# Performance work log

Measured on AMD Instinct MI355X. Metric: run time of the kernel, lower is better.

The kernel has to match this reference:

```python
import jax, jax.numpy as jnp
import numpy as np

N_NODES = 100000
N_EDGES = 500000
NUM_REL = 1000  # static stand-in for rel.max()+1 (all relation ids appear w.h.p.)
E_HID, T_HID, R_HID = 256, 128, 128
NEG_SLOPE = 0.01  # F.leaky_relu default


def setup_inputs() -> dict:
    key = jax.random.key(0)
    ks = jax.random.split(key, 8)
    x_e = jax.random.normal(ks[0], (N_NODES, E_HID), dtype=jnp.float32)
    edge_index = jax.random.randint(ks[1], (2, N_EDGES), 0, N_NODES, dtype=jnp.int32)
    rel = jax.random.randint(ks[2], (N_EDGES,), 0, NUM_REL, dtype=jnp.int32)
    x_res1 = jax.random.normal(ks[3], (N_EDGES, R_HID), dtype=jnp.float32)
    rel_size = jnp.arange(N_EDGES, dtype=jnp.int32)  # column indices of the spmm
    s = 0.02
    W_tc1 = jax.random.normal(ks[4], (E_HID, T_HID), dtype=jnp.float32) * s
    b_tc1 = jnp.zeros((T_HID,), dtype=jnp.float32)
    W_sr1 = jax.random.normal(ks[5], (2 * T_HID, R_HID), dtype=jnp.float32) * s
    b_sr1 = jnp.zeros((R_HID,), dtype=jnp.float32)
    a1 = jax.random.normal(ks[6], (R_HID,), dtype=jnp.float32) * s
    a5 = jax.random.normal(ks[7], (R_HID,), dtype=jnp.float32) * s
    return {"x_e": x_e, "x_res1": x_res1, "W_tc1": W_tc1, "b_tc1": b_tc1,
            "W_sr1": W_sr1, "b_sr1": b_sr1, "a1": a1, "a5": a5,
            "edge_index": edge_index, "rel": rel, "rel_size": rel_size}


def reference(x_e, x_res1, W_tc1, b_tc1, W_sr1, b_sr1, a1, a5, edge_index, rel, rel_size):
    # t_c1: project node features to t_hidden
    s_t = x_e @ W_tc1 + b_tc1                      # [N, t]
    h = s_t[edge_index[0]]                          # [E, t] head features
    t = s_t[edge_index[1]]                          # [E, t] tail features

    # Per-relation mean of head/tail features (in torch this overwrites r_in_t,
    # which aliases r_in_t1, so downstream uses the means).
    counts = jax.ops.segment_sum(jnp.ones_like(rel, dtype=jnp.float32), rel,
                                 num_segments=NUM_REL)
    denom = jnp.maximum(counts, 1.0)[:, None]       # [R, 1]
    mean_h = jax.ops.segment_sum(h, rel, num_segments=NUM_REL) / denom  # [R, t]
    mean_t = jax.ops.segment_sum(t, rel, num_segments=NUM_REL) / denom  # [R, t]
    r_in_t1 = jnp.concatenate([mean_h[rel], mean_t[rel]], axis=1)       # [E, 2t]

    # s_r1 projection and attention logits
    x_res2 = r_in_t1 @ W_sr1 + b_sr1                # [E, r]
    e1 = x_res2 @ a1 + x_res1 @ a5                  # [E]
    e1 = jnp.where(e1 >= 0, e1, NEG_SLOPE * e1)     # leaky_relu

    # scatter-softmax grouped by rel
    seg_max = jax.ops.segment_max(e1, rel, num_segments=NUM_REL)
    ex = jnp.exp(e1 - seg_max[rel])
    seg_sum = jax.ops.segment_sum(ex, rel, num_segments=NUM_REL)
    alpha = ex / seg_sum[rel]                       # [E]

    # spmm: sparse [R, E] with (row=rel, col=rel_size, val=alpha) times x_res2
    x_type = jax.ops.segment_sum(alpha[:, None] * x_res2[rel_size], rel,
                                 num_segments=NUM_REL)  # [R, r]

    out_res = x_res1 + x_type[rel]                  # [E, r]
    return jnp.concatenate([out_res, r_in_t1], axis=1)  # [E, r + 2t]
```

## Files before the change

kernel.cpp:

```cpp
#include <hip/hip_runtime.h>

#define N_NODES_C 100000
#define N_EDGES_C 500000
#define NUM_REL_C 1000
#define E_HID_C   256
#define RPAD      1024

#define NB_SORT   125
#define CHUNK_E   (N_EDGES_C / NB_SORT)


__global__ __launch_bounds__(1024)
void k_zero(int* __restrict__ cnt) {
    cnt[threadIdx.x] = 0;
}

__global__ __launch_bounds__(1024)
void k_hist(const int* __restrict__ rel, int* __restrict__ part,
            int* __restrict__ cnt) {
    __shared__ int h[RPAD];
    const int b = blockIdx.x, tid = threadIdx.x;
    h[tid] = 0;
    __syncthreads();
    const int base = b * CHUNK_E;
    for (int e = base + tid; e < base + CHUNK_E; e += 1024)
        atomicAdd(&h[rel[e]], 1);
    __syncthreads();
    const int v = h[tid];
    part[b * RPAD + tid] = v;
    if (v) atomicAdd(&cnt[tid], v);
}

__global__ __launch_bounds__(1024)
void k_scan(const int* __restrict__ cnt, int* __restrict__ startc) {
    __shared__ int s[2][RPAD];
    const int t = threadIdx.x;
    const int v = cnt[t];
    s[0][t] = v;
    __syncthreads();
    int cur = 0;
    for (int off = 1; off < RPAD; off <<= 1) {
        const int add = (t >= off) ? s[cur][t - off] : 0;
        s[cur ^ 1][t] = s[cur][t] + add;
        cur ^= 1;
        __syncthreads();
    }
    startc[t] = s[cur][t] - v;
}

__global__ __launch_bounds__(64)
void k_pbase(const int* __restrict__ part, const int* __restrict__ startc,
             int* __restrict__ pbase) {
    const int r = blockIdx.x * 64 + threadIdx.x;
    int run = startc[r];
#pragma unroll 5
    for (int b = 0; b < NB_SORT; ++b) {
        pbase[b * RPAD + r] = run;
        run += part[b * RPAD + r];
    }
}

__global__ __launch_bounds__(1024)
void k_scatter(const int* __restrict__ edge_index, const int* __restrict__ rel,
               const int* __restrict__ pbase,
               int* __restrict__ bsrc, int* __restrict__ bdst) {
    __shared__ int cur[RPAD];
    const int b = blockIdx.x, tid = threadIdx.x;
    cur[tid] = pbase[b * RPAD + tid];
    __syncthreads();
    const int base = b * CHUNK_E;
    for (int e = base + tid; e < base + CHUNK_E; e += 1024) {
        const int r = rel[e];
        const int pos = atomicAdd(&cur[r], 1);
        bsrc[pos] = edge_index[e];
        bdst[pos] = edge_index[N_EDGES_C + e];
    }
}

__global__ __launch_bounds__(512)
void k_accum(const float* __restrict__ x_e,
             const int* __restrict__ bsrc, const int* __restrict__ bdst,
             const int* __restrict__ startc, const int* __restrict__ cnt,
             const float* __restrict__ W_tc1, const float* __restrict__ b_tc1,
             const float* __restrict__ W_sr1, const float* __restrict__ b_sr1,
             float* __restrict__ rin_t,
             float* __restrict__ xt_t)
{
    __shared__ float red[8][E_HID_C];
    __shared__ float mh[E_HID_C], mt[E_HID_C], rin[E_HID_C];
    const int r    = blockIdx.x;
    const int tid  = threadIdx.x;
    const int w    = tid >> 6;
    const int lane = tid & 63;
    const int which = w >> 2;
    const int q     = w & 3;
    const int base = startc[r];
    const int c    = cnt[r];
    const int qlen = (c + 3) >> 2;
    const int lo = base + q * qlen;
    const int hi = min(base + c, lo + qlen);
    const int* __restrict__ bn = which ? bdst : bsrc;

    float4 a = make_float4(0.f, 0.f, 0.f, 0.f);
    for (int g = lo; g < hi; g += 64) {
        const int m = min(64, hi - g);
        const int myidx = (g + lane < hi) ? bn[g + lane] : 0;
        int k = 0;
        for (; k + 8 <= m; k += 8) {
            float4 v[8];
#pragma unroll
            for (int u = 0; u < 8; ++u) {
                const int n = __shfl(myidx, k + u);
                v[u] = ((const float4*)(x_e + (size_t)n * E_HID_C))[lane];
            }
#pragma unroll
            for (int u = 0; u < 8; ++u) {
                a.x += v[u].x; a.y += v[u].y; a.z += v[u].z; a.w += v[u].w;
            }
        }
        for (; k < m; ++k) {
            const int n = __shfl(myidx, k);
            const float4 v = ((const float4*)(x_e + (size_t)n * E_HID_C))[lane];
            a.x += v.x; a.y += v.y; a.z += v.z; a.w += v.w;
        }
    }

    ((float4*)&red[w][0])[lane] = a;
    __syncthreads();

    {
        const float inv = 1.0f / (float)(c > 0 ? c : 1);
        const int wh = tid >> 8;
        const int d  = tid & 255;
        const float s = red[wh * 4 + 0][d] + red[wh * 4 + 1][d] +
                        red[wh * 4 + 2][d] + red[wh * 4 + 3][d];
        (wh ? mt : mh)[d] = s * inv;
    }
    __syncthreads();

    if (tid < 256) {
        const int j = tid & 127;
        const float* __restrict__ src = (tid < 128) ? mh : mt;
        float acc = b_tc1[j];
        for (int k = 0; k < E_HID_C; ++k)
            acc += src[k] * W_tc1[k * 128 + j];
        rin[(tid < 128 ? 0 : 128) + j] = acc;
    }
    __syncthreads();

    if (tid < 256) {
        rin_t[(size_t)r * E_HID_C + tid] = rin[tid];
    } else if (tid < 384) {
        const int d = tid - 256;
        float acc = b_sr1[d];
        for (int k = 0; k < E_HID_C; ++k)
            acc += rin[k] * W_sr1[k * 128 + d];
        xt_t[(size_t)r * 128 + d] = acc;
    }
}

__global__ __launch_bounds__(256)
void k_out(const float* __restrict__ x_res1,
           const int* __restrict__ rel,
           const float* __restrict__ rin_t,
           const float* __restrict__ xt_t,
           float4* __restrict__ out)
{
    const float4* __restrict__ xr4  = (const float4*)x_res1;
    const float4* __restrict__ rin4 = (const float4*)rin_t;
    const float4* __restrict__ xt4  = (const float4*)xt_t;
    const int tid = threadIdx.x;
    const unsigned jj = tid & 31;
    const unsigned e  = blockIdx.x * 8u + (tid >> 5);
    const int r = rel[e];
    const float4 a = xr4[(size_t)e * 32 + jj];
    const float4 t = xt4[(size_t)r * 32 + jj];
    float4 o;
    o.x = a.x + t.x; o.y = a.y + t.y; o.z = a.z + t.z; o.w = a.w + t.w;
    float4* __restrict__ dst = out + (size_t)e * 96;
    dst[jj]      = o;
    dst[32 + jj] = rin4[(size_t)r * 64 + jj];
    dst[64 + jj] = rin4[(size_t)r * 64 + 32 + jj];
}

extern "C" void kernel_launch(void* const* d_in, const int* in_sizes, int n_in,
                              void* d_out, int out_size, void* d_ws, size_t ws_size,
                              hipStream_t stream)
{
    const float* x_e    = (const float*)d_in[0];
    const float* x_res1 = (const float*)d_in[1];
    const float* W_tc1  = (const float*)d_in[2];
    const float* b_tc1  = (const float*)d_in[3];
    const float* W_sr1  = (const float*)d_in[4];
    const float* b_sr1  = (const float*)d_in[5];
    const int* edge_index = (const int*)d_in[8];
    const int* rel        = (const int*)d_in[9];

    char* ws = (char*)d_ws;
    int*   part   = (int*)  (ws);
    int*   pbase  = (int*)  (ws + 512000);
    int*   cnt    = (int*)  (ws + 1024000);
    int*   startc = (int*)  (ws + 1028096);
    int*   bsrc   = (int*)  (ws + 1032192);
    int*   bdst   = (int*)  (ws + 3032192);
    float* rin_t  = (float*)(ws + 5032192);
    float* xt_t   = (float*)(ws + 6056192);

    k_zero   <<<1, RPAD, 0, stream>>>(cnt);
    k_hist   <<<NB_SORT, 1024, 0, stream>>>(rel, part, cnt);
    k_scan   <<<1, RPAD, 0, stream>>>(cnt, startc);
    k_pbase  <<<RPAD / 64, 64, 0, stream>>>(part, startc, pbase);
    k_scatter<<<NB_SORT, 1024, 0, stream>>>(edge_index, rel, pbase, bsrc, bdst);
    k_accum  <<<NUM_REL_C, 512, 0, stream>>>(x_e, bsrc, bdst, startc, cnt,
                                             W_tc1, b_tc1, W_sr1, b_sr1,
                                             rin_t, xt_t);
    k_out    <<<N_EDGES_C / 8, 256, 0, stream>>>(x_res1, rel, rin_t, xt_t,
                                                 (float4*)d_out);
}
```

Measured before the change: 381.8 us.

## Gather bf16 copy of node features, pack edge pairs, nontemporal output

Converts x_e to bf16 inside the histogram kernel when workspace allows, so the per-relation gather reads half the bytes per row; the gather unroll also grows from 8 to 16. Source and destination indices are packed into one int2 array, and the output kernel uses nontemporal loads and stores. The conversion is an extra full streaming pass over x_e (about 102 MB read, 51 MB written) that must be paid back by the cheaper random gathers. Summing bf16-rounded inputs also loses precision in the means.

```diff
diff --git a/kernel.cpp b/kernel.cpp
--- a/kernel.cpp
+++ b/kernel.cpp
@@ -8,7 +8,18 @@
 
 #define NB_SORT   125
 #define CHUNK_E   (N_EDGES_C / NB_SORT)
-
+#define NB_HIST   250
+#define XE_F4     (N_NODES_C * E_HID_C / 4)
+#define CONV_PER_BLK (XE_F4 / NB_HIST)
+
+
+typedef float f4 __attribute__((ext_vector_type(4)));
+
+__device__ __forceinline__ unsigned short bf16rne(float f) {
+    unsigned u = __float_as_uint(f);
+    u += 0x7FFFu + ((u >> 16) & 1u);
+    return (unsigned short)(u >> 16);
+}
 
 __global__ __launch_bounds__(1024)
 void k_zero(int* __restrict__ cnt) {
@@ -16,19 +27,35 @@
 }
 
 __global__ __launch_bounds__(1024)
-void k_hist(const int* __restrict__ rel, int* __restrict__ part,
-            int* __restrict__ cnt) {
+void k_hist(const int* __restrict__ rel, const float4* __restrict__ xe4,
+            int* __restrict__ part, int* __restrict__ cnt,
+            ushort4* __restrict__ xb4, const int do_conv) {
     __shared__ int h[RPAD];
     const int b = blockIdx.x, tid = threadIdx.x;
-    h[tid] = 0;
-    __syncthreads();
-    const int base = b * CHUNK_E;
-    for (int e = base + tid; e < base + CHUNK_E; e += 1024)
-        atomicAdd(&h[rel[e]], 1);
-    __syncthreads();
-    const int v = h[tid];
-    part[b * RPAD + tid] = v;
-    if (v) atomicAdd(&cnt[tid], v);
+    const bool hist = (b < NB_SORT);
+    if (hist) {
+        h[tid] = 0;
+        __syncthreads();
+        const int base = b * CHUNK_E;
+        for (int e = base + tid; e < base + CHUNK_E; e += 1024)
+            atomicAdd(&h[rel[e]], 1);
+    }
+    if (do_conv) {
+        const int cb = b * CONV_PER_BLK;
+        for (int i = cb + tid; i < cb + CONV_PER_BLK; i += 1024) {
+            const float4 v = xe4[i];
+            ushort4 o;
+            o.x = bf16rne(v.x); o.y = bf16rne(v.y);
+            o.z = bf16rne(v.z); o.w = bf16rne(v.w);
+            xb4[i] = o;
+        }
+    }
+    if (hist) {
+        __syncthreads();
+        const int c = h[tid];
+        part[b * RPAD + tid] = c;
+        if (c) atomicAdd(&cnt[tid], c);
+    }
 }
 
 __global__ __launch_bounds__(1024)
@@ -62,8 +89,7 @@
 
 __global__ __launch_bounds__(1024)
 void k_scatter(const int* __restrict__ edge_index, const int* __restrict__ rel,
-               const int* __restrict__ pbase,
-               int* __restrict__ bsrc, int* __restrict__ bdst) {
+               const int* __restrict__ pbase, int2* __restrict__ bpair) {
     __shared__ int cur[RPAD];
     const int b = blockIdx.x, tid = threadIdx.x;
     cur[tid] = pbase[b * RPAD + tid];
@@ -72,14 +98,14 @@
     for (int e = base + tid; e < base + CHUNK_E; e += 1024) {
         const int r = rel[e];
         const int pos = atomicAdd(&cur[r], 1);
-        bsrc[pos] = edge_index[e];
-        bdst[pos] = edge_index[N_EDGES_C + e];
-    }
-}
-
+        bpair[pos] = make_int2(edge_index[e], edge_index[N_EDGES_C + e]);
+    }
+}
+
+template<bool BF16>
 __global__ __launch_bounds__(512)
-void k_accum(const float* __restrict__ x_e,
-             const int* __restrict__ bsrc, const int* __restrict__ bdst,
+void k_accum(const float* __restrict__ x_e, const unsigned short* __restrict__ xb,
+             const int2* __restrict__ bp,
              const int* __restrict__ startc, const int* __restrict__ cnt,
              const float* __restrict__ W_tc1, const float* __restrict__ b_tc1,
              const float* __restrict__ W_sr1, const float* __restrict__ b_sr1,
@@ -99,29 +125,56 @@
     const int qlen = (c + 3) >> 2;
     const int lo = base + q * qlen;
     const int hi = min(base + c, lo + qlen);
-    const int* __restrict__ bn = which ? bdst : bsrc;
 
     float4 a = make_float4(0.f, 0.f, 0.f, 0.f);
     for (int g = lo; g < hi; g += 64) {
         const int m = min(64, hi - g);
-        const int myidx = (g + lane < hi) ? bn[g + lane] : 0;
+        int2 pr = make_int2(0, 0);
+        if (g + lane < hi) pr = bp[g + lane];
+        const int myidx = which ? pr.y : pr.x;
         int k = 0;
-        for (; k + 8 <= m; k += 8) {
-            float4 v[8];
-#pragma unroll
-            for (int u = 0; u < 8; ++u) {
-                const int n = __shfl(myidx, k + u);
-                v[u] = ((const float4*)(x_e + (size_t)n * E_HID_C))[lane];
-            }
-#pragma unroll
-            for (int u = 0; u < 8; ++u) {
-                a.x += v[u].x; a.y += v[u].y; a.z += v[u].z; a.w += v[u].w;
-            }
-        }
-        for (; k < m; ++k) {
-            const int n = __shfl(myidx, k);
-            const float4 v = ((const float4*)(x_e + (size_t)n * E_HID_C))[lane];
-            a.x += v.x; a.y += v.y; a.z += v.z; a.w += v.w;
+        if (BF16) {
+            for (; k + 16 <= m; k += 16) {
+                uint2 v[16];
+#pragma unroll
+                for (int u = 0; u < 16; ++u) {
+                    const int n = __shfl(myidx, k + u);
+                    v[u] = ((const uint2*)(xb + (size_t)n * E_HID_C))[lane];
+                }
+#pragma unroll
+                for (int u = 0; u < 16; ++u) {
+                    a.x += __uint_as_float(v[u].x << 16);
+                    a.y += __uint_as_float(v[u].x & 0xFFFF0000u);
+                    a.z += __uint_as_float(v[u].y << 16);
+                    a.w += __uint_as_float(v[u].y & 0xFFFF0000u);
+                }
+            }
+            for (; k < m; ++k) {
+                const int n = __shfl(myidx, k);
+                const uint2 v = ((const uint2*)(xb + (size_t)n * E_HID_C))[lane];
+                a.x += __uint_as_float(v.x << 16);
+                a.y += __uint_as_float(v.x & 0xFFFF0000u);
+                a.z += __uint_as_float(v.y << 16);
+                a.w += __uint_as_float(v.y & 0xFFFF0000u);
+            }
+        } else {
+            for (; k + 8 <= m; k += 8) {
+                float4 v[8];
+#pragma unroll
+                for (int u = 0; u < 8; ++u) {
+                    const int n = __shfl(myidx, k + u);
+                    v[u] = ((const float4*)(x_e + (size_t)n * E_HID_C))[lane];
+                }
+#pragma unroll
+                for (int u = 0; u < 8; ++u) {
+                    a.x += v[u].x; a.y += v[u].y; a.z += v[u].z; a.w += v[u].w;
+                }
+            }
+            for (; k < m; ++k) {
+                const int n = __shfl(myidx, k);
+                const float4 v = ((const float4*)(x_e + (size_t)n * E_HID_C))[lane];
+                a.x += v.x; a.y += v.y; a.z += v.z; a.w += v.w;
+            }
         }
     }
 
@@ -164,23 +217,22 @@
            const int* __restrict__ rel,
            const float* __restrict__ rin_t,
            const float* __restrict__ xt_t,
-           float4* __restrict__ out)
+           float* __restrict__ out)
 {
-    const float4* __restrict__ xr4  = (const float4*)x_res1;
-    const float4* __restrict__ rin4 = (const float4*)rin_t;
-    const float4* __restrict__ xt4  = (const float4*)xt_t;
+    const f4* __restrict__ xr4  = (const f4*)x_res1;
+    const f4* __restrict__ rin4 = (const f4*)rin_t;
+    const f4* __restrict__ xt4  = (const f4*)xt_t;
+    f4* __restrict__ o4 = (f4*)out;
     const int tid = threadIdx.x;
     const unsigned jj = tid & 31;
     const unsigned e  = blockIdx.x * 8u + (tid >> 5);
     const int r = rel[e];
-    const float4 a = xr4[(size_t)e * 32 + jj];
-    const float4 t = xt4[(size_t)r * 32 + jj];
-    float4 o;
-    o.x = a.x + t.x; o.y = a.y + t.y; o.z = a.z + t.z; o.w = a.w + t.w;
-    float4* __restrict__ dst = out + (size_t)e * 96;
-    dst[jj]      = o;
-    dst[32 + jj] = rin4[(size_t)r * 64 + jj];
-    dst[64 + jj] = rin4[(size_t)r * 64 + 32 + jj];
+    const f4 a = __builtin_nontemporal_load(&xr4[(size_t)e * 32 + jj]);
+    const f4 t = xt4[(size_t)r * 32 + jj];
+    f4* __restrict__ dst = o4 + (size_t)e * 96;
+    __builtin_nontemporal_store(a + t, &dst[jj]);
+    __builtin_nontemporal_store(rin4[(size_t)r * 64 + jj],      &dst[32 + jj]);
+    __builtin_nontemporal_store(rin4[(size_t)r * 64 + 32 + jj], &dst[64 + jj]);
 }
 
 extern "C" void kernel_launch(void* const* d_in, const int* in_sizes, int n_in,
@@ -201,19 +253,29 @@
     int*   pbase  = (int*)  (ws + 512000);
     int*   cnt    = (int*)  (ws + 1024000);
     int*   startc = (int*)  (ws + 1028096);
-    int*   bsrc   = (int*)  (ws + 1032192);
-    int*   bdst   = (int*)  (ws + 3032192);
+    int2*  bpair  = (int2*) (ws + 1032192);
     float* rin_t  = (float*)(ws + 5032192);
     float* xt_t   = (float*)(ws + 6056192);
+    unsigned short* xb = (unsigned short*)(ws + 6568192);
+    const size_t need_bf16 = 6568192ull + 51200000ull;
+    const bool use_bf16 = (ws_size >= need_bf16);
 
     k_zero   <<<1, RPAD, 0, stream>>>(cnt);
-    k_hist   <<<NB_SORT, 1024, 0, stream>>>(rel, part, cnt);
+    k_hist   <<<use_bf16 ? NB_HIST : NB_SORT, 1024, 0, stream>>>(
+                 rel, (const float4*)x_e, part, cnt,
+                 (ushort4*)xb, use_bf16 ? 1 : 0);
     k_scan   <<<1, RPAD, 0, stream>>>(cnt, startc);
     k_pbase  <<<RPAD / 64, 64, 0, stream>>>(part, startc, pbase);
-    k_scatter<<<NB_SORT, 1024, 0, stream>>>(edge_index, rel, pbase, bsrc, bdst);
-    k_accum  <<<NUM_REL_C, 512, 0, stream>>>(x_e, bsrc, bdst, startc, cnt,
-                                             W_tc1, b_tc1, W_sr1, b_sr1,
-                                             rin_t, xt_t);
+    k_scatter<<<NB_SORT, 1024, 0, stream>>>(edge_index, rel, pbase, bpair);
+    if (use_bf16) {
+        k_accum<true><<<NUM_REL_C, 512, 0, stream>>>(
+            x_e, xb, bpair, startc, cnt,
+            W_tc1, b_tc1, W_sr1, b_sr1, rin_t, xt_t);
+    } else {
+        k_accum<false><<<NUM_REL_C, 512, 0, stream>>>(
+            x_e, xb, bpair, startc, cnt,
+            W_tc1, b_tc1, W_sr1, b_sr1, rin_t, xt_t);
+    }
     k_out    <<<N_EDGES_C / 8, 256, 0, stream>>>(x_res1, rel, rin_t, xt_t,
-                                                 (float4*)d_out);
-}
+                                                 (float*)d_out);
+}
```

After: 318.4 us. -16.6%, faster.
